# Performance work log

Measured on AMD Instinct MI355X. Metric: run time of the kernel, lower is better.

The kernel has to match this reference:

```python
import jax, jax.numpy as jnp
import numpy as np

B, FEAT, H, W = 16, 64, 32, 32


def setup_inputs() -> dict:
    key = jax.random.key(0)
    ks = jax.random.split(key, 8)
    s = 0.05
    return {
        "x": jax.random.normal(ks[0], (B, 2 * FEAT, H, W), jnp.float32),
        # i2s_conv: MaskConv(2F -> 4F, 1x1, maskB with group=1 == all-ones), bias=False
        "w_i2s": jax.random.normal(ks[1], (4 * FEAT, 2 * FEAT), jnp.float32) * s,
        # left/right state-to-state Conv2d(F -> 4F, kernel (2,1)), with bias
        "w_left": jax.random.normal(ks[2], (4 * FEAT, FEAT, 2), jnp.float32) * s,
        "b_left": jax.random.normal(ks[3], (4 * FEAT,), jnp.float32) * s,
        "w_right": jax.random.normal(ks[4], (4 * FEAT, FEAT, 2), jnp.float32) * s,
        "b_right": jax.random.normal(ks[5], (4 * FEAT,), jnp.float32) * s,
        # skip_conv: MaskConv(F -> 2F, 1x1, maskB group=1 == plain conv), bias=True
        "w_skip": jax.random.normal(ks[6], (2 * FEAT, FEAT), jnp.float32) * s,
        "b_skip": jax.random.normal(ks[7], (2 * FEAT,), jnp.float32) * s,
    }


def _shift_right_w(a):  # F.pad(a,(1,0,...))[..., :-1]
    return jnp.pad(a, ((0, 0), (0, 0), (0, 0), (1, 0)))[:, :, :, :-1]


def _shift_left_w(a):  # F.pad(a,(0,1,...))[..., 1:]
    return jnp.pad(a, ((0, 0), (0, 0), (0, 0), (0, 1)))[:, :, :, 1:]


def _shift_down_h(a):  # pad one row on top, drop last row
    return jnp.pad(a, ((0, 0), (0, 0), (1, 0), (0, 0)))[:, :, :-1, :]


def _s2s(hprev, w, b, wshift):
    # pad(top=1, side=1) + Conv2d kernel (2,1) + crop one column, expressed as
    # two 1x1 contractions on width-shifted / (width+height)-shifted maps.
    hw = wshift(hprev)            # [B,F,H,W] shifted one column
    hd = _shift_down_h(hw)        # additionally shifted one row down
    return (jnp.einsum('bchw,oc->bohw', hd, w[:, :, 0])
            + jnp.einsum('bchw,oc->bohw', hw, w[:, :, 1])
            + b[None, :, None, None])


def _forward(x, w_i2s, w_left, b_left, w_right, b_right, w_skip, b_skip):
    b_, c2, h_, w_ = x.shape
    f = c2 // 2
    hmap = jnp.einsum('bchw,oc->bohw', x, w_i2s)  # [B,4F,H,W]
    left_h = hmap   # stew: input-to-state shared between directions
    right_h = hmap
    zeros = jnp.zeros((b_, f, h_, w_), x.dtype)

    def step(carry, _):
        lc, lh, rc, rh = carry
        pre = jax.nn.sigmoid(_s2s(lh, w_left, b_left, _shift_right_w) + left_h)
        o, fg, ig, g = jnp.split(pre, 4, axis=1)
        lc = fg * lc + ig * g
        lh = o * jnp.tanh(lc)
        pre = jax.nn.sigmoid(_s2s(rh, w_right, b_right, _shift_left_w) + right_h)
        o, fg, ig, g = jnp.split(pre, 4, axis=1)
        rc = fg * rc + ig * g
        rh = o * jnp.tanh(rc)
        return (lc, lh, rc, rh), None

    (lc, lh, rc, rh), _ = jax.lax.scan(step, (zeros, zeros, zeros, zeros), None, length=h_)
    rh = _shift_down_h(rh)  # unstew + shift right stream down one row
    out_h = lh + rh         # [B,F,H,W]
    skip = jnp.einsum('bchw,oc->bohw', out_h, w_skip) + b_skip[None, :, None, None]
    return x + skip


def reference(x, w_i2s, w_left, b_left, w_right, b_right, w_skip, b_skip):
    return _forward(x, w_i2s, w_left, b_left, w_right, b_right, w_skip, b_skip)
```

## Files before the change

### kernel.cpp

```cpp
#include <hip/hip_runtime.h>


using bf16   = __bf16;
using bf16x8 = __attribute__((ext_vector_type(8))) __bf16;
using f32x4  = __attribute__((ext_vector_type(4))) float;

#define SCOPE_AGENT __HIP_MEMORY_SCOPE_AGENT

__device__ __forceinline__ bf16x8 bzero8() {
  bf16x8 v;
#pragma unroll
  for (int e = 0; e < 8; ++e) v[e] = (bf16)0.0f;
  return v;
}
__device__ __forceinline__ unsigned short f2bu(float f) {
  bf16 b = (bf16)f;
  return __builtin_bit_cast(unsigned short, b);
}
__device__ __forceinline__ float bu2f(unsigned short u) {
  return __uint_as_float(((unsigned)u) << 16);
}
__device__ __forceinline__ float sigf(float x) {
  return __builtin_amdgcn_rcpf(1.0f + __expf(-x));
}
__device__ __forceinline__ float tanh_fast(float x) {
  return 2.0f * __builtin_amdgcn_rcpf(1.0f + __expf(-2.0f * x)) - 1.0f;
}

__global__ void prep_kernel(const float* __restrict__ w_i2s,
                            const float* __restrict__ w_left,
                            const float* __restrict__ w_right,
                            const float* __restrict__ w_skip,
                            bf16* __restrict__ WnI, bf16* __restrict__ WnL,
                            bf16* __restrict__ WnR, bf16* __restrict__ WnS) {
  int t = blockIdx.x * 256 + threadIdx.x;
  if (t < 32768) {
    WnI[t] = (bf16)w_i2s[t];
    int o = t >> 7, k = t & 127;
    int src = (k < 64) ? (o * 128 + k * 2) : (o * 128 + (k - 64) * 2 + 1);
    WnL[t] = (bf16)w_left[src];
    WnR[t] = (bf16)w_right[src];
    if (t < 8192) WnS[t] = (bf16)w_skip[t];
  }
}

__global__ __launch_bounds__(256, 2)
void hmap_kernel(const float* __restrict__ x, const bf16* __restrict__ Wn,
                 ushort4* __restrict__ hmap2) {
  __shared__ __align__(16) bf16 At[64 * 128];
  const int tile = blockIdx.x;
  const int b = tile >> 4, h0 = (tile & 15) << 1;
  const int t = threadIdx.x;
  const float* xb = x + (size_t)(b * 128) * 1024 + h0 * 32;
#pragma unroll
  for (int i = 0; i < 8; ++i) {
    int idx = t + 256 * i;
    int cc = idx >> 4, m4 = idx & 15;
    f32x4 v = *(const f32x4*)(xb + (size_t)cc * 1024 + m4 * 4);
#pragma unroll
    for (int e = 0; e < 4; ++e) {
      int m = m4 * 4 + e;
      int kb = (cc * 2) ^ ((m & 7) << 4);
      *(bf16*)((char*)At + m * 256 + kb) = (bf16)v[e];
    }
  }
  __syncthreads();
  const int wv = t >> 6, l = t & 63;
  const int l15 = l & 15, lq = l >> 4;
  const int c = wv * 16 + l15;
  bf16x8 bfrag[4][4];
#pragma unroll
  for (int q = 0; q < 4; ++q)
#pragma unroll
    for (int kk = 0; kk < 4; ++kk)
      bfrag[q][kk] = *(const bf16x8*)(Wn + (q * 64 + c) * 128 + kk * 32 + lq * 8);
  f32x4 acc[4][4];
  const f32x4 fz = {0.f, 0.f, 0.f, 0.f};
#pragma unroll
  for (int ms = 0; ms < 4; ++ms)
#pragma unroll
    for (int q = 0; q < 4; ++q) acc[ms][q] = fz;
#pragma unroll
  for (int kk = 0; kk < 4; ++kk) {
#pragma unroll
    for (int ms = 0; ms < 4; ++ms) {
      int m = ms * 16 + l15;
      int kb = ((kk * 32 + lq * 8) * 2) ^ ((m & 7) << 4);
      bf16x8 a = *(const bf16x8*)((const char*)At + m * 256 + kb);
#pragma unroll
      for (int q = 0; q < 4; ++q)
        acc[ms][q] =
            __builtin_amdgcn_mfma_f32_16x16x32_bf16(a, bfrag[q][kk], acc[ms][q], 0, 0, 0);
    }
  }
  const int pix0 = tile * 64;
#pragma unroll
  for (int ms = 0; ms < 4; ++ms)
#pragma unroll
    for (int j = 0; j < 4; ++j) {
      int p = pix0 + ms * 16 + lq * 4 + j;
      ushort4 hv;
      hv.x = f2bu(acc[ms][0][j]);
      hv.y = f2bu(acc[ms][1][j]);
      hv.z = f2bu(acc[ms][2][j]);
      hv.w = f2bu(acc[ms][3][j]);
      hmap2[(size_t)p * 64 + c] = hv;
    }
}

__global__ __launch_bounds__(256, 2)
void scan_kernel(bf16* __restrict__ lhLout, bf16* __restrict__ lhRout,
                 const ushort4* __restrict__ hmap2,
                 const bf16* __restrict__ WnL, const bf16* __restrict__ WnR,
                 const float* __restrict__ bL, const float* __restrict__ bR,
                 bf16* __restrict__ ring, unsigned* __restrict__ prodFlag,
                 unsigned* __restrict__ consFlag) {
  __shared__ __align__(16) bf16 buf[2][3 * 32 * 64];
  const int blk = blockIdx.x;
  const int q = blk & 31, tl = blk >> 5;
  const bool right = (q & 1) != 0;
  const int b = q >> 1;
  const int r0 = tl * 2;
  const int t = threadIdx.x;
  const int dw = right ? 1 : -1;
  bf16* __restrict__ lout = right ? lhRout : lhLout;
  const bf16* __restrict__ Wn = right ? WnR : WnL;
  const float* __restrict__ bias = right ? bR : bL;
  const int wv = t >> 6, l = t & 63, l15 = l & 15, lq = l >> 4;
  const int c = wv * 16 + l15;

#pragma unroll
  for (int i = 0; i < 3; ++i) ((bf16x8*)buf[0])[t + 256 * i] = bzero8();
  ((bf16x8*)buf[1])[t] = bzero8();

  bf16x8 bfrag[4][4];
#pragma unroll
  for (int g = 0; g < 4; ++g)
#pragma unroll
    for (int kk = 0; kk < 4; ++kk)
      bfrag[g][kk] = *(const bf16x8*)(Wn + (g * 64 + c) * 128 + kk * 32 + lq * 8);
  float bq[4];
#pragma unroll
  for (int g = 0; g < 4; ++g) bq[g] = bias[g * 64 + c];
  ushort4 hmp[4][4];
#pragma unroll
  for (int ms = 0; ms < 4; ++ms)
#pragma unroll
    for (int j = 0; j < 4; ++j) {
      int w = (ms & 1) * 16 + lq * 4 + j;
      size_t p = (size_t)((b * 32 + r0 + (ms >> 1)) * 32 + w);
      hmp[ms][j] = hmap2[p * 64 + c];
    }
  float lc_r[4][4];
#pragma unroll
  for (int ms = 0; ms < 4; ++ms)
#pragma unroll
    for (int j = 0; j < 4; ++j) lc_r[ms][j] = 0.0f;

  const unsigned* pBelow = prodFlag + (size_t)(blk - 32) * 32;
  const unsigned* cAbove = consFlag + (size_t)(blk + 32) * 32;
  unsigned* myProd = prodFlag + (size_t)blk * 32;
  unsigned* myCons = consFlag + (size_t)blk * 32;

  __syncthreads();

  for (int s = 0; s < 32; ++s) {
    bf16* curb = buf[s & 1];
    bf16* nxtb = buf[(s + 1) & 1];
    const bool consume = (tl > 0) && (s > 0);
    const bool publish = (tl < 15) && (s < 31);
    bf16* slotOut = ring + (size_t)(((s & 7) * 512) + blk) * 2048;

    if (publish && s >= 8) {
      const unsigned tgt = (unsigned)(s - 7);
      while (__hip_atomic_load(cAbove, __ATOMIC_RELAXED, SCOPE_AGENT) < tgt)
        __builtin_amdgcn_s_sleep(1);
    }

#pragma unroll
    for (int ms = 2; ms < 4; ++ms) {
      const int wb_ = (ms & 1) * 16;
      const int wsrc = wb_ + l15 + dw;
      const bool oob = (unsigned)wsrc >= 32u;
      const int wc = wsrc & 31;
      f32x4 acc[4];
      const f32x4 fz = {0.f, 0.f, 0.f, 0.f};
#pragma unroll
      for (int g = 0; g < 4; ++g) acc[g] = fz;
#pragma unroll
      for (int kk = 0; kk < 4; ++kk) {
        const int srcr = 1 + (kk >> 1);
        const int c0 = (kk & 1) * 32 + lq * 8;
        int aoff = ((srcr * 32 + wc) * 128 + c0 * 2) ^ ((wc & 7) << 4);
        bf16x8 a = *(const bf16x8*)((const char*)curb + aoff);
        if (oob) a = bzero8();
#pragma unroll
        for (int g = 0; g < 4; ++g)
          acc[g] = __builtin_amdgcn_mfma_f32_16x16x32_bf16(a, bfrag[g][kk], acc[g], 0, 0, 0);
      }
#pragma unroll
      for (int j = 0; j < 4; ++j) {
        const int w = wb_ + lq * 4 + j;
        ushort4 hm = hmp[ms][j];
        float e0 = __expf(-(acc[0][j] + bu2f(hm.x) + bq[0]));
        float e1 = __expf(-(acc[1][j] + bu2f(hm.y) + bq[1]));
        float e2 = __expf(-(acc[2][j] + bu2f(hm.z) + bq[2]));
        float e3 = __expf(-(acc[3][j] + bu2f(hm.w) + bq[3]));
        float fg = __builtin_amdgcn_rcpf(1.0f + e1);
        float igg = __builtin_amdgcn_rcpf((1.0f + e2) * (1.0f + e3));
        float lcv = fg * lc_r[ms][j] + igg;
        lc_r[ms][j] = lcv;
        float ey = __expf(-2.0f * lcv);
        float lh = (1.0f - ey) * __builtin_amdgcn_rcpf((1.0f + e0) * (1.0f + ey));
        bf16 vb = (bf16)lh;
        int woff = ((2 * 32 + w) * 128 + c * 2) ^ ((w & 7) << 4);
        *(bf16*)((char*)nxtb + woff) = vb;
        if (publish) {
          unsigned u = (unsigned)__builtin_bit_cast(unsigned short, vb);
          unsigned pv = (unsigned)__shfl_xor((int)u, 1);
          if ((l & 1) == 0) {
            unsigned dword = u | (pv << 16);
            __hip_atomic_store((unsigned*)(slotOut + w * 64 + (c & ~1)), dword,
                               __ATOMIC_RELAXED, SCOPE_AGENT);
          }
        }
      }
    }
    __syncthreads();
    if (publish && t == 0)
      __hip_atomic_store(myProd, (unsigned)(s + 1), __ATOMIC_RELAXED, SCOPE_AGENT);

    if (consume) {
      const unsigned tgt = (unsigned)s;
      while (__hip_atomic_load(pBelow, __ATOMIC_RELAXED, SCOPE_AGENT) < tgt)
        __builtin_amdgcn_s_sleep(1);
      const bf16* slotIn =
          ring + (size_t)((((s - 1) & 7) * 512) + (blk - 32)) * 2048;
      int w = t >> 3, c8 = t & 7;
      const unsigned long long* src =
          (const unsigned long long*)(slotIn + w * 64 + c8 * 8);
      unsigned long long d0 = __hip_atomic_load(src, __ATOMIC_RELAXED, SCOPE_AGENT);
      unsigned long long d1 = __hip_atomic_load(src + 1, __ATOMIC_RELAXED, SCOPE_AGENT);
      int off = (w * 128 + c8 * 16) ^ ((w & 7) << 4);
      *(unsigned long long*)((char*)curb + off) = d0;
      *(unsigned long long*)((char*)curb + off + 8) = d1;
    }
    __syncthreads();
    if (consume && t == 0)
      __hip_atomic_store(myCons, (unsigned)s, __ATOMIC_RELAXED, SCOPE_AGENT);

#pragma unroll
    for (int ms = 0; ms < 2; ++ms) {
      const int wb_ = (ms & 1) * 16;
      const int wsrc = wb_ + l15 + dw;
      const bool oob = (unsigned)wsrc >= 32u;
      const int wc = wsrc & 31;
      f32x4 acc[4];
      const f32x4 fz = {0.f, 0.f, 0.f, 0.f};
#pragma unroll
      for (int g = 0; g < 4; ++g) acc[g] = fz;
#pragma unroll
      for (int kk = 0; kk < 4; ++kk) {
        const int srcr = kk >> 1;
        const int c0 = (kk & 1) * 32 + lq * 8;
        int aoff = ((srcr * 32 + wc) * 128 + c0 * 2) ^ ((wc & 7) << 4);
        bf16x8 a = *(const bf16x8*)((const char*)curb + aoff);
        if (oob) a = bzero8();
#pragma unroll
        for (int g = 0; g < 4; ++g)
          acc[g] = __builtin_amdgcn_mfma_f32_16x16x32_bf16(a, bfrag[g][kk], acc[g], 0, 0, 0);
      }
#pragma unroll
      for (int j = 0; j < 4; ++j) {
        const int w = wb_ + lq * 4 + j;
        ushort4 hm = hmp[ms][j];
        float e0 = __expf(-(acc[0][j] + bu2f(hm.x) + bq[0]));
        float e1 = __expf(-(acc[1][j] + bu2f(hm.y) + bq[1]));
        float e2 = __expf(-(acc[2][j] + bu2f(hm.z) + bq[2]));
        float e3 = __expf(-(acc[3][j] + bu2f(hm.w) + bq[3]));
        float fg = __builtin_amdgcn_rcpf(1.0f + e1);
        float igg = __builtin_amdgcn_rcpf((1.0f + e2) * (1.0f + e3));
        float lcv = fg * lc_r[ms][j] + igg;
        lc_r[ms][j] = lcv;
        float ey = __expf(-2.0f * lcv);
        float lh = (1.0f - ey) * __builtin_amdgcn_rcpf((1.0f + e0) * (1.0f + ey));
        int woff = ((1 * 32 + w) * 128 + c * 2) ^ ((w & 7) << 4);
        *(bf16*)((char*)nxtb + woff) = (bf16)lh;
      }
    }
    __syncthreads();
  }

#pragma unroll
  for (int i = 0; i < 2; ++i) {
    int idx = t + 256 * i;
    int R = 1 + (idx >> 8), rem = idx & 255;
    int w = rem >> 3, c8 = rem & 7;
    int off = ((R * 32 + w) * 128 + c8 * 16) ^ ((w & 7) << 4);
    bf16x8 v = *(const bf16x8*)((const char*)buf[0] + off);
    *(bf16x8*)(lout + (size_t)((b * 32 + r0 + R - 1) * 32 + w) * 64 + c8 * 8) = v;
  }
}

__global__ __launch_bounds__(256, 2)
void final_kernel(const float* __restrict__ x, const bf16* __restrict__ lhL,
                  const bf16* __restrict__ lhR, const bf16* __restrict__ Wn,
                  const float* __restrict__ b_skip, float* __restrict__ out) {
  __shared__ __align__(16) bf16 At[64 * 64];
  __shared__ __align__(16) float smemT[128 * 72];
  const int tile = blockIdx.x;
  const int b = tile >> 4, h0 = (tile & 15) << 1;
  const int t = threadIdx.x;
#pragma unroll
  for (int i = 0; i < 2; ++i) {
    int idx = t + 256 * i;
    int m = idx >> 3, c8 = idx & 7;
    int h = h0 + (m >> 5), w = m & 31;
    size_t p = (size_t)(b * 32 + h) * 32 + w;
    bf16x8 vL = *(const bf16x8*)(lhL + p * 64 + c8 * 8);
    bf16x8 v;
    if (h > 0) {
      bf16x8 vR = *(const bf16x8*)(lhR + (p - 32) * 64 + c8 * 8);
#pragma unroll
      for (int e = 0; e < 8; ++e) v[e] = (bf16)((float)vL[e] + (float)vR[e]);
    } else {
      v = vL;
    }
    int kb = (c8 * 16) ^ ((m & 7) << 4);
    *(bf16x8*)((char*)At + m * 128 + kb) = v;
  }
  __syncthreads();
  const int wv = t >> 6, l = t & 63;
  const int l15 = l & 15, lq = l >> 4;
  const int c = wv * 16 + l15;
  bf16x8 bfrag[2][2];
#pragma unroll
  for (int g = 0; g < 2; ++g)
#pragma unroll
    for (int kk = 0; kk < 2; ++kk)
      bfrag[g][kk] = *(const bf16x8*)(Wn + (g * 64 + c) * 64 + kk * 32 + lq * 8);
  f32x4 acc[4][2];
  const f32x4 fz = {0.f, 0.f, 0.f, 0.f};
#pragma unroll
  for (int ms = 0; ms < 4; ++ms)
#pragma unroll
    for (int g = 0; g < 2; ++g) acc[ms][g] = fz;
#pragma unroll
  for (int kk = 0; kk < 2; ++kk) {
#pragma unroll
    for (int ms = 0; ms < 4; ++ms) {
      int m = ms * 16 + l15;
      int kb = ((kk * 32 + lq * 8) * 2) ^ ((m & 7) << 4);
      bf16x8 a = *(const bf16x8*)((const char*)At + m * 128 + kb);
#pragma unroll
      for (int g = 0; g < 2; ++g)
        acc[ms][g] =
            __builtin_amdgcn_mfma_f32_16x16x32_bf16(a, bfrag[g][kk], acc[ms][g], 0, 0, 0);
    }
  }
  float bsk[2];
#pragma unroll
  for (int g = 0; g < 2; ++g) bsk[g] = b_skip[g * 64 + c];
#pragma unroll
  for (int ms = 0; ms < 4; ++ms)
#pragma unroll
    for (int g = 0; g < 2; ++g)
#pragma unroll
      for (int j = 0; j < 4; ++j) {
        int m = ms * 16 + lq * 4 + j;
        int n = g * 64 + c;
        smemT[n * 72 + m] = acc[ms][g][j] + bsk[g];
      }
  __syncthreads();
  const float* xb = x + (size_t)(b * 128) * 1024 + h0 * 32;
  float* ob = out + (size_t)(b * 128) * 1024 + h0 * 32;
#pragma unroll
  for (int i = 0; i < 8; ++i) {
    int idx = t + 256 * i;
    int o2 = idx >> 4, m4 = idx & 15;
    f32x4 s = *(const f32x4*)(&smemT[o2 * 72 + m4 * 4]);
    f32x4 xv = *(const f32x4*)(xb + (size_t)o2 * 1024 + m4 * 4);
#pragma unroll
    for (int e = 0; e < 4; ++e) s[e] += xv[e];
    *(f32x4*)(ob + (size_t)o2 * 1024 + m4 * 4) = s;
  }
}

extern "C" void kernel_launch(void* const* d_in, const int* in_sizes, int n_in,
                              void* d_out, int out_size, void* d_ws, size_t ws_size,
                              hipStream_t stream) {
  const float* x       = (const float*)d_in[0];
  const float* w_i2s   = (const float*)d_in[1];
  const float* w_left  = (const float*)d_in[2];
  const float* b_left  = (const float*)d_in[3];
  const float* w_right = (const float*)d_in[4];
  const float* b_right = (const float*)d_in[5];
  const float* w_skip  = (const float*)d_in[6];
  const float* b_skip  = (const float*)d_in[7];
  float* out = (float*)d_out;
  char* ws = (char*)d_ws;

  bf16*     lhL   = (bf16*)(ws + 0x0000000);
  bf16*     lhR   = (bf16*)(ws + 0x0200000);
  ushort4*  hmap2 = (ushort4*)(ws + 0x0400000);
  bf16*     ring  = (bf16*)(ws + 0x0C00000);
  unsigned* prodF = (unsigned*)(ws + 0x1C00000);
  unsigned* consF = (unsigned*)(ws + 0x1C10000);
  bf16*     WnI   = (bf16*)(ws + 0x1C20000);
  bf16*     WnL   = (bf16*)(ws + 0x1C30000);
  bf16*     WnR   = (bf16*)(ws + 0x1C40000);
  bf16*     WnS   = (bf16*)(ws + 0x1C50000);

  hipMemsetAsync(ws + 0x1C00000, 0, 0x20000, stream);
  prep_kernel<<<128, 256, 0, stream>>>(w_i2s, w_left, w_right, w_skip, WnI, WnL, WnR, WnS);
  hmap_kernel<<<256, 256, 0, stream>>>(x, WnI, hmap2);
  scan_kernel<<<512, 256, 0, stream>>>(lhL, lhR, hmap2, WnL, WnR,
                                       b_left, b_right, ring, prodF, consF);
  final_kernel<<<256, 256, 0, stream>>>(x, lhL, lhR, WnS, b_skip, out);
}
```

Measured before the change: 176.8 us.

## Split scan block work across 8 waves and fold log2e into weights

The scan kernel now launches 512 threads per block instead of 256. The two 16-column halves of each row go to separate wave groups, so each thread handles one m-subtile per row instead of two. This shortens each thread's serial per-step chain and halves its register state, at the cost of more waves per block and heavier barriers. Separately, log2(e) is pre-multiplied into the recurrent weights, biases and hmap, so the gates can use the native exp2 instruction instead of __expf's extra multiply.

```diff
diff --git a/kernel.cpp b/kernel.cpp
--- a/kernel.cpp
+++ b/kernel.cpp
@@ -6,6 +6,8 @@
 using f32x4  = __attribute__((ext_vector_type(4))) float;
 
 #define SCOPE_AGENT __HIP_MEMORY_SCOPE_AGENT
+#define LOG2E 1.4426950408889634f
+#define K2E   2.8853900817779268f
 
 __device__ __forceinline__ bf16x8 bzero8() {
   bf16x8 v;
@@ -19,12 +21,6 @@
 }
 __device__ __forceinline__ float bu2f(unsigned short u) {
   return __uint_as_float(((unsigned)u) << 16);
-}
-__device__ __forceinline__ float sigf(float x) {
-  return __builtin_amdgcn_rcpf(1.0f + __expf(-x));
-}
-__device__ __forceinline__ float tanh_fast(float x) {
-  return 2.0f * __builtin_amdgcn_rcpf(1.0f + __expf(-2.0f * x)) - 1.0f;
 }
 
 __global__ void prep_kernel(const float* __restrict__ w_i2s,
@@ -38,8 +34,8 @@
     WnI[t] = (bf16)w_i2s[t];
     int o = t >> 7, k = t & 127;
     int src = (k < 64) ? (o * 128 + k * 2) : (o * 128 + (k - 64) * 2 + 1);
-    WnL[t] = (bf16)w_left[src];
-    WnR[t] = (bf16)w_right[src];
+    WnL[t] = (bf16)(w_left[src] * LOG2E);
+    WnR[t] = (bf16)(w_right[src] * LOG2E);
     if (t < 8192) WnS[t] = (bf16)w_skip[t];
   }
 }
@@ -100,15 +96,15 @@
     for (int j = 0; j < 4; ++j) {
       int p = pix0 + ms * 16 + lq * 4 + j;
       ushort4 hv;
-      hv.x = f2bu(acc[ms][0][j]);
-      hv.y = f2bu(acc[ms][1][j]);
-      hv.z = f2bu(acc[ms][2][j]);
-      hv.w = f2bu(acc[ms][3][j]);
+      hv.x = f2bu(acc[ms][0][j] * LOG2E);
+      hv.y = f2bu(acc[ms][1][j] * LOG2E);
+      hv.z = f2bu(acc[ms][2][j] * LOG2E);
+      hv.w = f2bu(acc[ms][3][j] * LOG2E);
       hmap2[(size_t)p * 64 + c] = hv;
     }
 }
 
-__global__ __launch_bounds__(256, 2)
+__global__ __launch_bounds__(512, 4)
 void scan_kernel(bf16* __restrict__ lhLout, bf16* __restrict__ lhRout,
                  const ushort4* __restrict__ hmap2,
                  const bf16* __restrict__ WnL, const bf16* __restrict__ WnR,
@@ -126,12 +122,17 @@
   bf16* __restrict__ lout = right ? lhRout : lhLout;
   const bf16* __restrict__ Wn = right ? WnR : WnL;
   const float* __restrict__ bias = right ? bR : bL;
-  const int wv = t >> 6, l = t & 63, l15 = l & 15, lq = l >> 4;
+  const int w8 = t >> 6, l = t & 63, l15 = l & 15, lq = l >> 4;
+  const int wv = w8 & 3, mhalf = w8 >> 2;
   const int c = wv * 16 + l15;
-
-#pragma unroll
-  for (int i = 0; i < 3; ++i) ((bf16x8*)buf[0])[t + 256 * i] = bzero8();
-  ((bf16x8*)buf[1])[t] = bzero8();
+  const int wb_ = mhalf * 16;
+
+#pragma unroll
+  for (int i = 0; i < 2; ++i) {
+    int idx = t + 512 * i;
+    if (idx < 768) ((bf16x8*)buf[0])[idx] = bzero8();
+  }
+  if (t < 256) ((bf16x8*)buf[1])[t] = bzero8();
 
   bf16x8 bfrag[4][4];
 #pragma unroll
@@ -141,29 +142,31 @@
       bfrag[g][kk] = *(const bf16x8*)(Wn + (g * 64 + c) * 128 + kk * 32 + lq * 8);
   float bq[4];
 #pragma unroll
-  for (int g = 0; g < 4; ++g) bq[g] = bias[g * 64 + c];
-  ushort4 hmp[4][4];
-#pragma unroll
-  for (int ms = 0; ms < 4; ++ms)
-#pragma unroll
-    for (int j = 0; j < 4; ++j) {
-      int w = (ms & 1) * 16 + lq * 4 + j;
-      size_t p = (size_t)((b * 32 + r0 + (ms >> 1)) * 32 + w);
-      hmp[ms][j] = hmap2[p * 64 + c];
-    }
-  float lc_r[4][4];
-#pragma unroll
-  for (int ms = 0; ms < 4; ++ms)
-#pragma unroll
-    for (int j = 0; j < 4; ++j) lc_r[ms][j] = 0.0f;
+  for (int g = 0; g < 4; ++g) bq[g] = bias[g * 64 + c] * LOG2E;
+  ushort4 hmpA[4], hmpB[4];
+  float lcA[4], lcB[4];
+#pragma unroll
+  for (int j = 0; j < 4; ++j) {
+    int w = wb_ + lq * 4 + j;
+    hmpA[j] = hmap2[(size_t)((b * 32 + r0 + 1) * 32 + w) * 64 + c];
+    hmpB[j] = hmap2[(size_t)((b * 32 + r0) * 32 + w) * 64 + c];
+    lcA[j] = 0.0f;
+    lcB[j] = 0.0f;
+  }
 
   const unsigned* pBelow = prodFlag + (size_t)(blk - 32) * 32;
   const unsigned* cAbove = consFlag + (size_t)(blk + 32) * 32;
   unsigned* myProd = prodFlag + (size_t)blk * 32;
   unsigned* myCons = consFlag + (size_t)blk * 32;
 
+  const int wsrc = wb_ + l15 + dw;
+  const bool oob = (unsigned)wsrc >= 32u;
+  const int wc = wsrc & 31;
+  const int swz = (wc & 7) << 4;
+
   __syncthreads();
 
+#pragma unroll 1
   for (int s = 0; s < 32; ++s) {
     bf16* curb = buf[s & 1];
     bf16* nxtb = buf[(s + 1) & 1];
@@ -177,12 +180,7 @@
         __builtin_amdgcn_s_sleep(1);
     }
 
-#pragma unroll
-    for (int ms = 2; ms < 4; ++ms) {
-      const int wb_ = (ms & 1) * 16;
-      const int wsrc = wb_ + l15 + dw;
-      const bool oob = (unsigned)wsrc >= 32u;
-      const int wc = wsrc & 31;
+    {
       f32x4 acc[4];
       const f32x4 fz = {0.f, 0.f, 0.f, 0.f};
 #pragma unroll
@@ -191,7 +189,7 @@
       for (int kk = 0; kk < 4; ++kk) {
         const int srcr = 1 + (kk >> 1);
         const int c0 = (kk & 1) * 32 + lq * 8;
-        int aoff = ((srcr * 32 + wc) * 128 + c0 * 2) ^ ((wc & 7) << 4);
+        int aoff = ((srcr * 32 + wc) * 128 + c0 * 2) ^ swz;
         bf16x8 a = *(const bf16x8*)((const char*)curb + aoff);
         if (oob) a = bzero8();
 #pragma unroll
@@ -201,16 +199,16 @@
 #pragma unroll
       for (int j = 0; j < 4; ++j) {
         const int w = wb_ + lq * 4 + j;
-        ushort4 hm = hmp[ms][j];
-        float e0 = __expf(-(acc[0][j] + bu2f(hm.x) + bq[0]));
-        float e1 = __expf(-(acc[1][j] + bu2f(hm.y) + bq[1]));
-        float e2 = __expf(-(acc[2][j] + bu2f(hm.z) + bq[2]));
-        float e3 = __expf(-(acc[3][j] + bu2f(hm.w) + bq[3]));
+        ushort4 hm = hmpA[j];
+        float e0 = __builtin_amdgcn_exp2f(-(acc[0][j] + bu2f(hm.x) + bq[0]));
+        float e1 = __builtin_amdgcn_exp2f(-(acc[1][j] + bu2f(hm.y) + bq[1]));
+        float e2 = __builtin_amdgcn_exp2f(-(acc[2][j] + bu2f(hm.z) + bq[2]));
+        float e3 = __builtin_amdgcn_exp2f(-(acc[3][j] + bu2f(hm.w) + bq[3]));
         float fg = __builtin_amdgcn_rcpf(1.0f + e1);
         float igg = __builtin_amdgcn_rcpf((1.0f + e2) * (1.0f + e3));
-        float lcv = fg * lc_r[ms][j] + igg;
-        lc_r[ms][j] = lcv;
-        float ey = __expf(-2.0f * lcv);
+        float lcv = fg * lcA[j] + K2E * igg;
+        lcA[j] = lcv;
+        float ey = __builtin_amdgcn_exp2f(-lcv);
         float lh = (1.0f - ey) * __builtin_amdgcn_rcpf((1.0f + e0) * (1.0f + ey));
         bf16 vb = (bf16)lh;
         int woff = ((2 * 32 + w) * 128 + c * 2) ^ ((w & 7) << 4);
@@ -234,27 +232,24 @@
       const unsigned tgt = (unsigned)s;
       while (__hip_atomic_load(pBelow, __ATOMIC_RELAXED, SCOPE_AGENT) < tgt)
         __builtin_amdgcn_s_sleep(1);
-      const bf16* slotIn =
-          ring + (size_t)((((s - 1) & 7) * 512) + (blk - 32)) * 2048;
-      int w = t >> 3, c8 = t & 7;
-      const unsigned long long* src =
-          (const unsigned long long*)(slotIn + w * 64 + c8 * 8);
-      unsigned long long d0 = __hip_atomic_load(src, __ATOMIC_RELAXED, SCOPE_AGENT);
-      unsigned long long d1 = __hip_atomic_load(src + 1, __ATOMIC_RELAXED, SCOPE_AGENT);
-      int off = (w * 128 + c8 * 16) ^ ((w & 7) << 4);
-      *(unsigned long long*)((char*)curb + off) = d0;
-      *(unsigned long long*)((char*)curb + off + 8) = d1;
+      if (t < 256) {
+        const bf16* slotIn =
+            ring + (size_t)((((s - 1) & 7) * 512) + (blk - 32)) * 2048;
+        int w = t >> 3, c8 = t & 7;
+        const unsigned long long* src =
+            (const unsigned long long*)(slotIn + w * 64 + c8 * 8);
+        unsigned long long d0 = __hip_atomic_load(src, __ATOMIC_RELAXED, SCOPE_AGENT);
+        unsigned long long d1 = __hip_atomic_load(src + 1, __ATOMIC_RELAXED, SCOPE_AGENT);
+        int off = (w * 128 + c8 * 16) ^ ((w & 7) << 4);
+        *(unsigned long long*)((char*)curb + off) = d0;
+        *(unsigned long long*)((char*)curb + off + 8) = d1;
+      }
     }
     __syncthreads();
     if (consume && t == 0)
       __hip_atomic_store(myCons, (unsigned)s, __ATOMIC_RELAXED, SCOPE_AGENT);
 
-#pragma unroll
-    for (int ms = 0; ms < 2; ++ms) {
-      const int wb_ = (ms & 1) * 16;
-      const int wsrc = wb_ + l15 + dw;
-      const bool oob = (unsigned)wsrc >= 32u;
-      const int wc = wsrc & 31;
+    {
       f32x4 acc[4];
       const f32x4 fz = {0.f, 0.f, 0.f, 0.f};
 #pragma unroll
@@ -263,7 +258,7 @@
       for (int kk = 0; kk < 4; ++kk) {
         const int srcr = kk >> 1;
         const int c0 = (kk & 1) * 32 + lq * 8;
-        int aoff = ((srcr * 32 + wc) * 128 + c0 * 2) ^ ((wc & 7) << 4);
+        int aoff = ((srcr * 32 + wc) * 128 + c0 * 2) ^ swz;
         bf16x8 a = *(const bf16x8*)((const char*)curb + aoff);
         if (oob) a = bzero8();
 #pragma unroll
@@ -273,16 +268,16 @@
 #pragma unroll
       for (int j = 0; j < 4; ++j) {
         const int w = wb_ + lq * 4 + j;
-        ushort4 hm = hmp[ms][j];
-        float e0 = __expf(-(acc[0][j] + bu2f(hm.x) + bq[0]));
-        float e1 = __expf(-(acc[1][j] + bu2f(hm.y) + bq[1]));
-        float e2 = __expf(-(acc[2][j] + bu2f(hm.z) + bq[2]));
-        float e3 = __expf(-(acc[3][j] + bu2f(hm.w) + bq[3]));
+        ushort4 hm = hmpB[j];
+        float e0 = __builtin_amdgcn_exp2f(-(acc[0][j] + bu2f(hm.x) + bq[0]));
+        float e1 = __builtin_amdgcn_exp2f(-(acc[1][j] + bu2f(hm.y) + bq[1]));
+        float e2 = __builtin_amdgcn_exp2f(-(acc[2][j] + bu2f(hm.z) + bq[2]));
+        float e3 = __builtin_amdgcn_exp2f(-(acc[3][j] + bu2f(hm.w) + bq[3]));
         float fg = __builtin_amdgcn_rcpf(1.0f + e1);
         float igg = __builtin_amdgcn_rcpf((1.0f + e2) * (1.0f + e3));
-        float lcv = fg * lc_r[ms][j] + igg;
-        lc_r[ms][j] = lcv;
-        float ey = __expf(-2.0f * lcv);
+        float lcv = fg * lcB[j] + K2E * igg;
+        lcB[j] = lcv;
+        float ey = __builtin_amdgcn_exp2f(-lcv);
         float lh = (1.0f - ey) * __builtin_amdgcn_rcpf((1.0f + e0) * (1.0f + ey));
         int woff = ((1 * 32 + w) * 128 + c * 2) ^ ((w & 7) << 4);
         *(bf16*)((char*)nxtb + woff) = (bf16)lh;
@@ -291,10 +286,8 @@
     __syncthreads();
   }
 
-#pragma unroll
-  for (int i = 0; i < 2; ++i) {
-    int idx = t + 256 * i;
-    int R = 1 + (idx >> 8), rem = idx & 255;
+  {
+    int R = 1 + (t >> 8), rem = t & 255;
     int w = rem >> 3, c8 = rem & 7;
     int off = ((R * 32 + w) * 128 + c8 * 16) ^ ((w & 7) << 4);
     bf16x8 v = *(const bf16x8*)((const char*)buf[0] + off);
@@ -414,7 +407,7 @@
   hipMemsetAsync(ws + 0x1C00000, 0, 0x20000, stream);
   prep_kernel<<<128, 256, 0, stream>>>(w_i2s, w_left, w_right, w_skip, WnI, WnL, WnR, WnS);
   hmap_kernel<<<256, 256, 0, stream>>>(x, WnI, hmap2);
-  scan_kernel<<<512, 256, 0, stream>>>(lhL, lhR, hmap2, WnL, WnR,
+  scan_kernel<<<512, 512, 0, stream>>>(lhL, lhR, hmap2, WnL, WnR,
                                        b_left, b_right, ring, prodF, consF);
   final_kernel<<<256, 256, 0, stream>>>(x, lhL, lhR, WnS, b_skip, out);
 }
```

Result: slower. 417.5 us (+136.2%).
